# Optimization experiments

Measured on AMD Instinct MI355X. Metric: run time of the kernel, lower is better.

The kernel has to match this reference:

```python
import jax, jax.numpy as jnp
import numpy as np

PS = 16          # patch_size
E = 256          # embed_dim
NH = 4           # num_heads
THR = 1.5        # entropy_threshold (bits)
LN_EPS = 1e-5


def _ln(x, g, b):
    m = x.mean(-1, keepdims=True)
    v = ((x - m) ** 2).mean(-1, keepdims=True)
    return (x - m) / jnp.sqrt(v + LN_EPS) * g + b


def _forward(video, conv_w, conv_b, wq_w, wq_b, wk_w, wk_b, wv_w, wv_b,
             lnq_g, lnq_b, lnk_g, lnk_b, lnv_g, lnv_b,
             in_proj_w, in_proj_b, out_proj_w, out_proj_b,
             dense_w, dense_b, bproj_w, bproj_b, group_query, ent_table):
    # Conv3d(3->E, k=(3,PS,PS), s=(2,PS,PS), p=(1,0,0)) + ReLU
    x = jax.lax.conv_general_dilated(
        video, conv_w, window_strides=(2, PS, PS),
        padding=((1, 1), (0, 0), (0, 0)),
        dimension_numbers=('NCDHW', 'OIDHW', 'NCDHW'))
    x = jax.nn.relu(x + conv_b[None, :, None, None, None])
    B = x.shape[0]
    tokens = x.reshape(B, E, -1).transpose(0, 2, 1)  # [B, N, E]
    N = tokens.shape[1]

    # per-token byte (no_grad in torch)
    byte = jax.lax.stop_gradient(
        jnp.clip(jnp.round(tokens.mean(-1) * 255.0), 0, 255)).astype(jnp.int32)  # [B, N]
    # entropy predictor: probs = softmax(ent_table[last_byte]) (last byte of running seq)
    logits = ent_table[byte[0]]                      # [N, 256]
    p = jax.nn.softmax(logits, axis=-1)
    ent = -(p * jnp.log2(p + 1e-9)).sum(-1)          # [N]
    boundary = (ent > THR).astype(jnp.int32)
    seg = jnp.cumsum(boundary) - boundary            # exclusive cumsum -> segment id per token

    # DecoderCrossAttention with a single shared group_query per segment
    q0 = jnp.broadcast_to(group_query, (B, 1, E))    # byte_representations
    query = _ln(q0 @ wq_w.T + wq_b, lnq_g, lnq_b)    # [B,1,E]
    k = _ln(tokens @ wk_w.T + wk_b, lnk_g, lnk_b)    # [B,N,E]
    v = _ln(tokens @ wv_w.T + wv_b, lnv_g, lnv_b)

    Wqi, Wki, Wvi = in_proj_w[:E], in_proj_w[E:2 * E], in_proj_w[2 * E:]
    bqi, bki, bvi = in_proj_b[:E], in_proj_b[E:2 * E], in_proj_b[2 * E:]
    dh = E // NH
    qp = ((query @ Wqi.T + bqi) * (dh ** -0.5)).reshape(B, NH, dh)  # [B,H,dh]
    kp = (k @ Wki.T + bki).reshape(B, N, NH, dh)
    vp = (v @ Wvi.T + bvi).reshape(B, N, NH, dh)

    scores = jnp.einsum('bhd,bnhd->nbh', qp, kp)     # [N,B,H]
    smax = jax.ops.segment_max(scores, seg, num_segments=N)   # [N,B,H]
    w = jnp.exp(scores - smax[seg])
    denom = jax.ops.segment_sum(w, seg, num_segments=N)       # [N,B,H]
    num = jax.ops.segment_sum(w[..., None] * vp.transpose(1, 0, 2, 3),
                              seg, num_segments=N)            # [N,B,H,dh]
    count = jax.ops.segment_sum(jnp.ones((N,), scores.dtype), seg, num_segments=N)
    valid = count > 0
    safe = jnp.where(valid[:, None, None], denom, 1.0)
    attn = (num / safe[..., None]).transpose(1, 0, 2, 3).reshape(B, N, E)
    out = attn @ out_proj_w.T + out_proj_b
    out = out @ dense_w.T + dense_b
    out = out + q0                                   # residual with byte_representations
    patches = out @ bproj_w.T + bproj_b              # binary_proj
    return jnp.where(valid[None, :, None], patches, 0.0)  # [B, N, E] padded


def setup_inputs() -> dict:
    key = jax.random.key(0)
    ks = jax.random.split(key, 16)
    rn = lambda k, s, sc=0.02: jax.random.normal(k, s, jnp.float32) * sc
    z = lambda *s: jnp.zeros(s, jnp.float32)
    o = lambda *s: jnp.ones(s, jnp.float32)
    return {
        'video': jax.random.normal(ks[0], (4, 3, 32, 224, 224), jnp.float32),
        'conv_w': rn(ks[1], (E, 3, 3, PS, PS)), 'conv_b': z(E),
        'wq_w': rn(ks[2], (E, E)), 'wq_b': z(E),
        'wk_w': rn(ks[3], (E, E)), 'wk_b': z(E),
        'wv_w': rn(ks[4], (E, E)), 'wv_b': z(E),
        'lnq_g': o(E), 'lnq_b': z(E),
        'lnk_g': o(E), 'lnk_b': z(E),
        'lnv_g': o(E), 'lnv_b': z(E),
        'in_proj_w': rn(ks[5], (3 * E, E)), 'in_proj_b': z(3 * E),
        'out_proj_w': rn(ks[6], (E, E)), 'out_proj_b': z(E),
        'dense_w': rn(ks[7], (E, E)), 'dense_b': z(E),
        'bproj_w': rn(ks[8], (E, E)), 'bproj_b': z(E),
        'group_query': jax.random.normal(ks[9], (1, 1, E), jnp.float32),
        'ent_table': jax.random.normal(ks[10], (256, 256), jnp.float32) * 6.0,
    }


def reference(video, conv_w, conv_b, wq_w, wq_b, wk_w, wk_b, wv_w, wv_b,
              lnq_g, lnq_b, lnk_g, lnk_b, lnv_g, lnv_b,
              in_proj_w, in_proj_b, out_proj_w, out_proj_b,
              dense_w, dense_b, bproj_w, bproj_b, group_query, ent_table):
    return _forward(video, conv_w, conv_b, wq_w, wq_b, wk_w, wk_b, wv_w, wv_b,
                    lnq_g, lnq_b, lnk_g, lnk_b, lnv_g, lnv_b,
                    in_proj_w, in_proj_b, out_proj_w, out_proj_b,
                    dense_w, dense_b, bproj_w, bproj_b, group_query, ent_table)
```

## Files before the change

kernel.cpp:

```cpp
#include <hip/hip_runtime.h>
#include <hip/hip_bf16.h>
#include <math.h>

#define NTOK 3136
#define MT 12544
#define KCV 2304
#define THRESH 1.5f
#define LN_EPS 1e-5f

typedef short short8 __attribute__((ext_vector_type(8)));
typedef float f32x4 __attribute__((ext_vector_type(4)));

__device__ __forceinline__ unsigned short f2bf(float f) {
    unsigned int u = __float_as_uint(f);
    u += 0x7fffu + ((u >> 16) & 1u);
    return (unsigned short)(u >> 16);
}
__device__ __forceinline__ float bf2f(unsigned short h) {
    return __uint_as_float(((unsigned int)h) << 16);
}
__device__ __forceinline__ unsigned int cvt_pk_bf16(float x0, float x1) {
    union { __hip_bfloat162 h; unsigned int u; } cv;
    cv.h = __float22bfloat162_rn(make_float2(x0, x1));
    return cv.u;
}
__device__ __forceinline__ void async16(const void* g, void* l) {
    __builtin_amdgcn_global_load_lds((const __attribute__((address_space(1))) void*)g,
                                     (__attribute__((address_space(3))) void*)l, 16, 0, 0);
}

__device__ __forceinline__ float wsum(float v) {
#pragma unroll
    for (int o = 32; o > 0; o >>= 1) v += __shfl_xor(v, o);
    return v;
}
__device__ __forceinline__ float wmax(float v) {
#pragma unroll
    for (int o = 32; o > 0; o >>= 1) v = fmaxf(v, __shfl_xor(v, o));
    return v;
}

__global__ __launch_bounds__(256) void prep_k(
    const float* __restrict__ cw, unsigned short* __restrict__ cwh,
    unsigned short* __restrict__ cwl,
    const float* __restrict__ s0, const float* __restrict__ s1, const float* __restrict__ s2,
    unsigned short* __restrict__ dst,
    const float* __restrict__ gq, const float* __restrict__ wq_w,
    const float* __restrict__ wq_b, const float* __restrict__ lnq_g,
    const float* __restrict__ lnq_b, const float* __restrict__ inW,
    const float* __restrict__ inB, float* __restrict__ qp,
    const float* __restrict__ Wd, const float* __restrict__ Wo,
    const float* __restrict__ bo, const float* __restrict__ bd,
    float* __restrict__ D1, float* __restrict__ tvec)
{
    const int blk = blockIdx.x;
    const int t = threadIdx.x;
    if (blk < 288) {
        int i = blk * 256 + t;
        int e = i & 255, kg = i >> 8;
        const float4* sp = (const float4*)(cw + (size_t)e * KCV + kg * 8);
        float4 x0 = sp[0], x1 = sp[1];
        float av[8] = {x0.x, x0.y, x0.z, x0.w, x1.x, x1.y, x1.z, x1.w};
        short8 hh, ll;
#pragma unroll
        for (int j = 0; j < 8; ++j) {
            unsigned short h = f2bf(av[j]);
            hh[j] = (short)h;
            ll[j] = (short)f2bf(av[j] - bf2f(h));
        }
        size_t off = (size_t)kg * 2048 + e * 8;
        *(short8*)&cwh[off] = hh;
        *(short8*)&cwl[off] = ll;
    } else if (blk < 1568) {
        int i = (blk - 288) * 256 + t;
        if (i >= 327680) return;
        float v;
        if      (i <  65536) v = s0[i];
        else if (i < 131072) v = s1[i - 65536];
        else                 v = s2[i - 131072];
        dst[i] = f2bf(v);
    } else if (blk == 1568) {
        __shared__ float sh[256];
        __shared__ float red[256];
        float acc = wq_b[t];
        for (int j = 0; j < 256; j++) acc += gq[j] * wq_w[t * 256 + j];
        red[t] = acc; __syncthreads();
        for (int o = 128; o > 0; o >>= 1) { if (t < o) red[t] += red[t + o]; __syncthreads(); }
        float m = red[0] * (1.f / 256.f);
        __syncthreads();
        float d = acc - m;
        red[t] = d * d; __syncthreads();
        for (int o = 128; o > 0; o >>= 1) { if (t < o) red[t] += red[t + o]; __syncthreads(); }
        float inv = 1.f / sqrtf(red[0] * (1.f / 256.f) + LN_EPS);
        sh[t] = d * inv * lnq_g[t] + lnq_b[t];
        __syncthreads();
        float a2 = inB[t];
        for (int j = 0; j < 256; j++) a2 += sh[j] * inW[t * 256 + j];
        qp[t] = a2 * 0.125f;
    } else if (blk < 1825) {
        int i = blk - 1569;
        float acc = 0.f;
        for (int k = 0; k < 256; k++) acc += Wd[i * 256 + k] * Wo[k * 256 + t];
        D1[i * 256 + t] = acc;
    } else {
        float acc = bd[t] + gq[t];
        for (int k = 0; k < 256; k++) acc += Wd[t * 256 + k] * bo[k];
        tvec[t] = acc;
    }
}

__global__ __launch_bounds__(256) void prep2_k(
    const float* __restrict__ Wb, const float* __restrict__ D1,
    const float* __restrict__ tvec, const float* __restrict__ bb,
    unsigned short* __restrict__ WcB, float* __restrict__ bc)
{
    const int blk = blockIdx.x;
    const int t = threadIdx.x;
    if (blk < 256) {
        int i = blk;
        float acc = 0.f;
        for (int k = 0; k < 256; k++) acc += Wb[i * 256 + k] * D1[k * 256 + t];
        WcB[i * 256 + t] = f2bf(acc);
    } else {
        float acc = bb[t];
        for (int k = 0; k < 256; k++) acc += Wb[t * 256 + k] * tvec[k];
        bc[t] = acc;
    }
}

__global__ __launch_bounds__(256) void conv_mfma_k(
    const float* __restrict__ video, const unsigned short* __restrict__ cwh,
    const unsigned short* __restrict__ cwl, const float* __restrict__ cbias,
    float* __restrict__ tokmean4, unsigned short* __restrict__ outB)
{
    __shared__ __align__(16) unsigned short Bh[8192], Bl[8192];
    const int t    = threadIdx.x;
    const int lane = t & 63;
    const int w    = t >> 6;
    const int l15  = lane & 15, lq = lane >> 4;
    const int v_  = blockIdx.x;
    const int s_  = (v_ & 7) * 98 + (v_ >> 3);
    const int mb  = s_ >> 2, eb = s_ & 3;
    const int m0  = mb * 64, e0 = eb * 64;

    const int m = m0 + w * 16 + l15;
    const int b = m / NTOK, n = m % NTOK;
    const int d = n / 196, hw = n % 196;
    const int h = hw / 14, ww = hw % 14;
    const float* vb = video + (size_t)(b * 3) * (32 * 50176) + (h * 16) * 224 + ww * 16;
    const int dbase = 2 * d - 1;

    f32x4 acc[4] = {};
    float4 a0, a1, a2, a3, b0, b1, b2, b3;
    short8 rh0, rh1, rl0, rl1;

#define BLOAD(s)                                                                     \
    {                                                                                \
        const size_t g0 = (size_t)((s) * 8 + w) * 2048 + (e0 + lane) * 8;            \
        const size_t g1 = g0 + 4 * 2048;                                             \
        rh0 = *(const short8*)(cwh + g0);                                            \
        rh1 = *(const short8*)(cwh + g1);                                            \
        rl0 = *(const short8*)(cwl + g0);                                            \
        rl1 = *(const short8*)(cwl + g1);                                            \
    }
#define BSTORE(buf)                                                                  \
    {                                                                                \
        const int o = (buf) * 4096 + w * 512 + lane * 8;                             \
        *(short8*)&Bh[o]        = rh0;                                               \
        *(short8*)&Bh[o + 2048] = rh1;                                               \
        *(short8*)&Bl[o]        = rl0;                                               \
        *(short8*)&Bl[o + 2048] = rl1;                                               \
    }
#define LOAD_A32(k0v, x0, x1)                                                        \
    {                                                                                \
        const int k0  = (k0v) + lq * 8;                                              \
        const int c   = k0 / 768;                                                    \
        const int rem = k0 - c * 768;                                                \
        const int kd  = rem >> 8;                                                    \
        const int r2  = rem & 255;                                                   \
        const int id  = dbase + kd;                                                  \
        x0 = make_float4(0.f, 0.f, 0.f, 0.f); x1 = x0;                               \
        if (id >= 0) {                                                               \
            const float* p = vb + (size_t)c * (32 * 50176) + id * 50176 +            \
                             (r2 >> 4) * 224 + (r2 & 15);                            \
            x0 = *(const float4*)p;                                                  \
            x1 = *(const float4*)(p + 4);                                            \
        }                                                                            \
    }
#define CVT_AB(y0, y1, fah, fal)                                                     \
    short8 fah, fal;                                                                 \
    {                                                                                \
        float av[8] = {y0.x, y0.y, y0.z, y0.w, y1.x, y1.y, y1.z, y1.w};              \
        unsigned int ph[4], pl[4];                                                   \
        _Pragma("unroll")                                                            \
        for (int j = 0; j < 4; ++j) {                                                \
            float u0 = av[2 * j], u1 = av[2 * j + 1];                                \
            unsigned int hu = cvt_pk_bf16(u0, u1);                                   \
            float r0 = u0 - __uint_as_float(hu << 16);                               \
            float r1 = u1 - __uint_as_float(hu & 0xffff0000u);                       \
            ph[j] = hu;                                                              \
            pl[j] = cvt_pk_bf16(r0, r1);                                             \
        }                                                                            \
        int4 phv = make_int4(ph[0], ph[1], ph[2], ph[3]);                            \
        int4 plv = make_int4(pl[0], pl[1], pl[2], pl[3]);                            \
        fah = *(short8*)&phv;                                                        \
        fal = *(short8*)&plv;                                                        \
    }

    BLOAD(0);
    LOAD_A32(0, a0, a1);
    LOAD_A32(32, a2, a3);
    BSTORE(0);
    __syncthreads();

    for (int s = 0; s < 36; ++s) {
        const int cbuf = s & 1;
        if (s + 1 < 36) {
            BLOAD(s + 1);
            LOAD_A32((s + 1) * 64,      b0, b1);
            LOAD_A32((s + 1) * 64 + 32, b2, b3);
        }
        {
            CVT_AB(a0, a1, fah, fal);
            const int rb = cbuf * 4096 + lq * 512 + l15 * 8;
#pragma unroll
            for (int ct = 0; ct < 4; ++ct) {
                short8 fbh = *(const short8*)&Bh[rb + ct * 128];
                short8 fbl = *(const short8*)&Bl[rb + ct * 128];
                acc[ct] = __builtin_amdgcn_mfma_f32_16x16x32_bf16(fah, fbh, acc[ct], 0, 0, 0);
                acc[ct] = __builtin_amdgcn_mfma_f32_16x16x32_bf16(fah, fbl, acc[ct], 0, 0, 0);
                acc[ct] = __builtin_amdgcn_mfma_f32_16x16x32_bf16(fal, fbh, acc[ct], 0, 0, 0);
            }
        }
        {
            CVT_AB(a2, a3, fah, fal);
            const int rb = cbuf * 4096 + (4 + lq) * 512 + l15 * 8;
#pragma unroll
            for (int ct = 0; ct < 4; ++ct) {
                short8 fbh = *(const short8*)&Bh[rb + ct * 128];
                short8 fbl = *(const short8*)&Bl[rb + ct * 128];
                acc[ct] = __builtin_amdgcn_mfma_f32_16x16x32_bf16(fah, fbh, acc[ct], 0, 0, 0);
                acc[ct] = __builtin_amdgcn_mfma_f32_16x16x32_bf16(fah, fbl, acc[ct], 0, 0, 0);
                acc[ct] = __builtin_amdgcn_mfma_f32_16x16x32_bf16(fal, fbh, acc[ct], 0, 0, 0);
            }
        }
        if (s + 1 < 36) BSTORE(cbuf ^ 1);
        __syncthreads();
        a0 = b0; a1 = b1; a2 = b2; a3 = b3;
    }
#undef BLOAD
#undef BSTORE
#undef LOAD_A32
#undef CVT_AB

    const int rbase = m0 + w * 16 + lq * 4;
    float rsum[4] = {0.f, 0.f, 0.f, 0.f};
#pragma unroll
    for (int ct = 0; ct < 4; ++ct) {
        int e = e0 + ct * 16 + l15;
        float bias = cbias[e];
#pragma unroll
        for (int r = 0; r < 4; ++r) {
            float vv = fmaxf(acc[ct][r] + bias, 0.f);
            outB[(size_t)(rbase + r) * 256 + e] = f2bf(vv);
            rsum[r] += vv;
        }
    }
    if (m0 < NTOK) {
#pragma unroll
        for (int r = 0; r < 4; ++r) {
            float sv = rsum[r];
            sv += __shfl_xor(sv, 1); sv += __shfl_xor(sv, 2);
            sv += __shfl_xor(sv, 4); sv += __shfl_xor(sv, 8);
            if (l15 == 0) tokmean4[(size_t)eb * NTOK + rbase + r] = sv;
        }
    }
}

__global__ __launch_bounds__(256) void gemm_single_k(
    const unsigned short* __restrict__ A, const unsigned short* __restrict__ W,
    const float* __restrict__ bias, const float* __restrict__ addvec,
    const int* __restrict__ Sptr, float* __restrict__ outF, unsigned short* __restrict__ outB)
{
    __shared__ __align__(16) unsigned short As[8192], Bs[8192];
    const int t = threadIdx.x, lane = t & 63, w = t >> 6;
    const int v_ = blockIdx.x;
    const int s_ = (v_ & 7) * 98 + (v_ >> 3);
    const int m0 = (s_ >> 2) * 64, e0 = (s_ & 3) * 64;
    const int l15 = lane & 15, lq = lane >> 4;
    const unsigned short* ga = A + (size_t)(m0 + lane) * 256;
    const unsigned short* gb = W + (size_t)(e0 + lane) * 256;
#pragma unroll
    for (int kg = w; kg < 16; kg += 4) {
        async16(ga + kg * 8, &As[kg * 512]);
        async16(gb + kg * 8, &Bs[kg * 512]);
    }
    f32x4 acc[4] = {};
    __syncthreads();
#pragma unroll
    for (int s = 0; s < 4; ++s) {
        int kg = s * 4 + lq;
        short8 a = *(const short8*)&As[kg * 512 + (w * 16 + l15) * 8];
#pragma unroll
        for (int ct = 0; ct < 4; ++ct) {
            short8 bb = *(const short8*)&Bs[kg * 512 + (ct * 16 + l15) * 8];
            acc[ct] = __builtin_amdgcn_mfma_f32_16x16x32_bf16(a, bb, acc[ct], 0, 0, 0);
        }
    }
    __syncthreads();
#pragma unroll
    for (int kg = w; kg < 16; kg += 4) {
        async16(ga + (16 + kg) * 8, &As[kg * 512]);
        async16(gb + (16 + kg) * 8, &Bs[kg * 512]);
    }
    __syncthreads();
#pragma unroll
    for (int s = 0; s < 4; ++s) {
        int kg = s * 4 + lq;
        short8 a = *(const short8*)&As[kg * 512 + (w * 16 + l15) * 8];
#pragma unroll
        for (int ct = 0; ct < 4; ++ct) {
            short8 bb = *(const short8*)&Bs[kg * 512 + (ct * 16 + l15) * 8];
            acc[ct] = __builtin_amdgcn_mfma_f32_16x16x32_bf16(a, bb, acc[ct], 0, 0, 0);
        }
    }
    int S = Sptr ? *Sptr : 0x7fffffff;
    int rbase = m0 + w * 16 + lq * 4;
#pragma unroll
    for (int ct = 0; ct < 4; ++ct) {
        int e = e0 + ct * 16 + l15;
        float bv = bias[e] + (addvec ? addvec[e] : 0.f);
#pragma unroll
        for (int r = 0; r < 4; ++r) {
            int mm = rbase + r;
            float vv = acc[ct][r] + bv;
            if ((mm % NTOK) >= S) vv = 0.f;
            size_t off = (size_t)mm * 256 + e;
            if (outF) outF[off] = vv;
            if (outB) outB[off] = f2bf(vv);
        }
    }
}

__global__ __launch_bounds__(256) void gemm_dual_k(
    const unsigned short* __restrict__ A0, const unsigned short* __restrict__ A1,
    const unsigned short* __restrict__ W,
    const float* __restrict__ bias0, const float* __restrict__ bias1,
    unsigned short* __restrict__ outB0, unsigned short* __restrict__ outB1)
{
    __shared__ __align__(16) unsigned short As[8192], Bs[8192];
    const int t = threadIdx.x, lane = t & 63, w = t >> 6;
    const int v_ = blockIdx.x;
    const int s_ = (v_ & 7) * 196 + (v_ >> 3);
    const int mb = s_ >> 3, ebg = s_ & 7;
    const int half = ebg >> 2;
    const unsigned short* A = half ? A1 : A0;
    const float* bias = half ? bias1 : bias0;
    unsigned short* outB = half ? outB1 : outB0;
    const int m0 = mb * 64, eg0 = ebg * 64, el0 = (ebg & 3) * 64;
    const int l15 = lane & 15, lq = lane >> 4;
    const unsigned short* ga = A + (size_t)(m0 + lane) * 256;
    const unsigned short* gb = W + (size_t)(eg0 + lane) * 256;
#pragma unroll
    for (int kg = w; kg < 16; kg += 4) {
        async16(ga + kg * 8, &As[kg * 512]);
        async16(gb + kg * 8, &Bs[kg * 512]);
    }
    f32x4 acc[4] = {};
    __syncthreads();
#pragma unroll
    for (int s = 0; s < 4; ++s) {
        int kg = s * 4 + lq;
        short8 a = *(const short8*)&As[kg * 512 + (w * 16 + l15) * 8];
#pragma unroll
        for (int ct = 0; ct < 4; ++ct) {
            short8 bb = *(const short8*)&Bs[kg * 512 + (ct * 16 + l15) * 8];
            acc[ct] = __builtin_amdgcn_mfma_f32_16x16x32_bf16(a, bb, acc[ct], 0, 0, 0);
        }
    }
    __syncthreads();
#pragma unroll
    for (int kg = w; kg < 16; kg += 4) {
        async16(ga + (16 + kg) * 8, &As[kg * 512]);
        async16(gb + (16 + kg) * 8, &Bs[kg * 512]);
    }
    __syncthreads();
#pragma unroll
    for (int s = 0; s < 4; ++s) {
        int kg = s * 4 + lq;
        short8 a = *(const short8*)&As[kg * 512 + (w * 16 + l15) * 8];
#pragma unroll
        for (int ct = 0; ct < 4; ++ct) {
            short8 bb = *(const short8*)&Bs[kg * 512 + (ct * 16 + l15) * 8];
            acc[ct] = __builtin_amdgcn_mfma_f32_16x16x32_bf16(a, bb, acc[ct], 0, 0, 0);
        }
    }
    int rbase = m0 + w * 16 + lq * 4;
#pragma unroll
    for (int ct = 0; ct < 4; ++ct) {
        int e = el0 + ct * 16 + l15;
        float bv = bias[e];
#pragma unroll
        for (int r = 0; r < 4; ++r) {
            float vv = acc[ct][r] + bv;
            outB[(size_t)(rbase + r) * 256 + e] = f2bf(vv);
        }
    }
}

__global__ __launch_bounds__(256, 2) void gemm_ln_k(
    const unsigned short* __restrict__ A0, const unsigned short* __restrict__ A1,
    const unsigned short* __restrict__ W,
    const float* __restrict__ bias0, const float* __restrict__ bias1,
    const float* __restrict__ g0, const float* __restrict__ b0,
    const float* __restrict__ g1, const float* __restrict__ b1,
    unsigned short* __restrict__ outVp, const float* __restrict__ qp,
    float* __restrict__ sc)
{
    __shared__ __align__(16) unsigned short As[16384], Bs[16384];
    __shared__ float pst[2][4][64];
    __shared__ float rmean[64], rinv[64];
    const int t = threadIdx.x, lane = t & 63, w = t >> 6;
    const int v_ = blockIdx.x;
    const int s_ = (v_ & 7) * 196 + (v_ >> 3);
    const int mb = s_ >> 3, ebg = s_ & 7;
    const int half = ebg >> 2;
    const unsigned short* A = half ? A1 : A0;
    const float* bias = half ? bias1 : bias0;
    const float* lng  = half ? g1 : g0;
    const float* lnb  = half ? b1 : b0;
    const int m0 = mb * 64, eg0 = ebg * 64, el0 = (ebg & 3) * 64;
    const int l15 = lane & 15, lq = lane >> 4;
    const unsigned short* ga = A + (size_t)(m0 + lane) * 256;
    const unsigned short* gb = W + (size_t)(eg0 + lane) * 256;
#pragma unroll
    for (int kg = w; kg < 32; kg += 4) {
        async16(ga + kg * 8, &As[kg * 512]);
        async16(gb + kg * 8, &Bs[kg * 512]);
    }
    __syncthreads();
    {
        float sum = 0.f, sq = 0.f;
#pragma unroll
        for (int k8 = 0; k8 < 8; ++k8) {
            short8 x = *(const short8*)&As[(w * 8 + k8) * 512 + lane * 8];
#pragma unroll
            for (int j = 0; j < 8; ++j) {
                float xv = bf2f((unsigned short)x[j]);
                sum += xv; sq += xv * xv;
            }
        }
        pst[0][w][lane] = sum; pst[1][w][lane] = sq;
    }
    __syncthreads();
    if (w == 0) {
        float s4 = (pst[0][0][lane] + pst[0][1][lane]) + (pst[0][2][lane] + pst[0][3][lane]);
        float q4 = (pst[1][0][lane] + pst[1][1][lane]) + (pst[1][2][lane] + pst[1][3][lane]);
        float mean = s4 * (1.f / 256.f);
        float var  = q4 * (1.f / 256.f) - mean * mean;
        rmean[lane] = mean;
        rinv[lane]  = 1.f / sqrtf(var + LN_EPS);
    }
    __syncthreads();
    const float myMean = rmean[w * 16 + l15];
    const float myInv  = rinv [w * 16 + l15];

    f32x4 acc[4] = {};
#pragma unroll
    for (int s = 0; s < 8; ++s) {
        int kg = s * 4 + lq;
        short8 araw = *(const short8*)&As[kg * 512 + (w * 16 + l15) * 8];
        float4 gA = *(const float4*)&lng[kg * 8];
        float4 gB = *(const float4*)&lng[kg * 8 + 4];
        float4 bA = *(const float4*)&lnb[kg * 8];
        float4 bB = *(const float4*)&lnb[kg * 8 + 4];
        float y[8];
        y[0] = (bf2f((unsigned short)araw[0]) - myMean) * myInv * gA.x + bA.x;
        y[1] = (bf2f((unsigned short)araw[1]) - myMean) * myInv * gA.y + bA.y;
        y[2] = (bf2f((unsigned short)araw[2]) - myMean) * myInv * gA.z + bA.z;
        y[3] = (bf2f((unsigned short)araw[3]) - myMean) * myInv * gA.w + bA.w;
        y[4] = (bf2f((unsigned short)araw[4]) - myMean) * myInv * gB.x + bB.x;
        y[5] = (bf2f((unsigned short)araw[5]) - myMean) * myInv * gB.y + bB.y;
        y[6] = (bf2f((unsigned short)araw[6]) - myMean) * myInv * gB.z + bB.z;
        y[7] = (bf2f((unsigned short)araw[7]) - myMean) * myInv * gB.w + bB.w;
        int4 pk = make_int4(cvt_pk_bf16(y[0], y[1]), cvt_pk_bf16(y[2], y[3]),
                            cvt_pk_bf16(y[4], y[5]), cvt_pk_bf16(y[6], y[7]));
        short8 a = *(short8*)&pk;
#pragma unroll
        for (int ct = 0; ct < 4; ++ct) {
            short8 bb = *(const short8*)&Bs[kg * 512 + (ct * 16 + l15) * 8];
            acc[ct] = __builtin_amdgcn_mfma_f32_16x16x32_bf16(a, bb, acc[ct], 0, 0, 0);
        }
    }
    int rbase = m0 + w * 16 + lq * 4;
    if (half == 0) {
        float sp[4] = {0.f, 0.f, 0.f, 0.f};
#pragma unroll
        for (int ct = 0; ct < 4; ++ct) {
            int e = el0 + ct * 16 + l15;
            float bv = bias[e];
            float qv = qp[e];
#pragma unroll
            for (int r = 0; r < 4; ++r) sp[r] += (acc[ct][r] + bv) * qv;
        }
#pragma unroll
        for (int r = 0; r < 4; ++r) {
            sp[r] += __shfl_xor(sp[r], 1); sp[r] += __shfl_xor(sp[r], 2);
            sp[r] += __shfl_xor(sp[r], 4); sp[r] += __shfl_xor(sp[r], 8);
        }
        if (l15 == 0) {
#pragma unroll
            for (int r = 0; r < 4; ++r) {
                int mm = rbase + r;
                int bb = mm / NTOK, nn = mm % NTOK;
                sc[(bb * 4 + ebg) * NTOK + nn] = sp[r];
            }
        }
    } else {
#pragma unroll
        for (int ct = 0; ct < 4; ++ct) {
            int e = el0 + ct * 16 + l15;
            float bv = bias[e];
#pragma unroll
            for (int r = 0; r < 4; ++r) {
                float vv = acc[ct][r] + bv;
                outVp[(size_t)(rbase + r) * 256 + e] = f2bf(vv);
            }
        }
    }
}

__global__ __launch_bounds__(256) void boundary_k(
    const float* __restrict__ tokmean4, const float* __restrict__ ent_table,
    int* __restrict__ boundary)
{
    int n    = blockIdx.x * 4 + (threadIdx.x >> 6);
    int lane = threadIdx.x & 63;
    float s0 = tokmean4[n];
    float s1 = tokmean4[NTOK + n];
    float s2 = tokmean4[2 * NTOK + n];
    float s3 = tokmean4[3 * NTOK + n];
    float mean = ((s0 + s1) + (s2 + s3)) * (1.f / 256.f);
    float bf = rintf(mean * 255.f);
    bf = fminf(fmaxf(bf, 0.f), 255.f);
    int byte = (int)bf;
    const float4 lg = reinterpret_cast<const float4*>(ent_table + byte * 256)[lane];
    float mx = wmax(fmaxf(fmaxf(lg.x, lg.y), fmaxf(lg.z, lg.w)));
    float e0 = expf(lg.x - mx), e1 = expf(lg.y - mx), e2 = expf(lg.z - mx), e3 = expf(lg.w - mx);
    float z = wsum(e0 + e1 + e2 + e3);
    float iz = 1.f / z;
    float p0 = e0 * iz, p1 = e1 * iz, p2 = e2 * iz, p3 = e3 * iz;
    float ep = -(p0 * log2f(p0 + 1e-9f) + p1 * log2f(p1 + 1e-9f) +
                 p2 * log2f(p2 + 1e-9f) + p3 * log2f(p3 + 1e-9f));
    ep = wsum(ep);
    if (lane == 0) boundary[n] = (ep > THRESH) ? 1 : 0;
}

__global__ __launch_bounds__(256) void scan_k(const int* __restrict__ boundary,
    int* __restrict__ seg_start, int* __restrict__ Sptr)
{
    __shared__ int sums[256];
    const int t = threadIdx.x;
    const int CH = 13;
    int base = t * CH;
    int s = 0;
    for (int i = 0; i < CH; i++) { int n = base + i; if (n < NTOK) s += boundary[n]; }
    sums[t] = s; __syncthreads();
    for (int o = 1; o < 256; o <<= 1) {
        int v = sums[t];
        int u = (t >= o) ? sums[t - o] : 0;
        __syncthreads();
        sums[t] = v + u;
        __syncthreads();
    }
    int run = (t == 0) ? 0 : sums[t - 1];
    if (t == 0) seg_start[0] = 0;
    for (int i = 0; i < CH; i++) {
        int n = base + i;
        if (n >= NTOK) break;
        int v = boundary[n];
        if (n == NTOK - 1) { Sptr[0] = run + 1; seg_start[run + 1] = NTOK; }
        if (v && (n + 1 < NTOK)) seg_start[run + 1] = n + 1;
        run += v;
    }
}

__global__ __launch_bounds__(256) void attn_bf_k(const float* __restrict__ sc,
    const unsigned short* __restrict__ vp, const int* __restrict__ seg_start,
    const int* __restrict__ Sptr, unsigned short* __restrict__ attn)
{
    int s    = blockIdx.x;
    int b    = blockIdx.y;
    int h    = threadIdx.x >> 6;
    int lane = threadIdx.x & 63;
    unsigned short* orow = attn + ((size_t)b * NTOK + s) * 256;
    int S = *Sptr;
    if (s >= S) { orow[h * 64 + lane] = 0; return; }
    int st = seg_start[s], en = seg_start[s + 1];
    const float* scr = sc + (b * 4 + h) * NTOK;
    float m = -1e30f;
    for (int n = st; n < en; n++) m = fmaxf(m, scr[n]);
    float den = 0.f, acc = 0.f;
    const unsigned short* vpb = vp + (size_t)b * NTOK * 256 + h * 64 + lane;
    for (int n = st; n < en; n++) {
        float wgt = expf(scr[n] - m);
        den += wgt;
        acc += wgt * bf2f(vpb[(size_t)n * 256]);
    }
    orow[h * 64 + lane] = f2bf(acc / den);
}

extern "C" void kernel_launch(void* const* d_in, const int* in_sizes, int n_in,
                              void* d_out, int out_size, void* d_ws, size_t ws_size,
                              hipStream_t stream)
{
    const float* video      = (const float*)d_in[0];
    const float* conv_w     = (const float*)d_in[1];
    const float* conv_b     = (const float*)d_in[2];
    const float* wq_w       = (const float*)d_in[3];
    const float* wq_b       = (const float*)d_in[4];
    const float* wk_w       = (const float*)d_in[5];
    const float* wk_b       = (const float*)d_in[6];
    const float* wv_w       = (const float*)d_in[7];
    const float* wv_b       = (const float*)d_in[8];
    const float* lnq_g      = (const float*)d_in[9];
    const float* lnq_b      = (const float*)d_in[10];
    const float* lnk_g      = (const float*)d_in[11];
    const float* lnk_b      = (const float*)d_in[12];
    const float* lnv_g      = (const float*)d_in[13];
    const float* lnv_b      = (const float*)d_in[14];
    const float* in_proj_w  = (const float*)d_in[15];
    const float* in_proj_b  = (const float*)d_in[16];
    const float* out_proj_w = (const float*)d_in[17];
    const float* out_proj_b = (const float*)d_in[18];
    const float* dense_w    = (const float*)d_in[19];
    const float* dense_b    = (const float*)d_in[20];
    const float* bproj_w    = (const float*)d_in[21];
    const float* bproj_b    = (const float*)d_in[22];
    const float* group_q    = (const float*)d_in[23];
    const float* ent_table  = (const float*)d_in[24];
    float* out = (float*)d_out;

    float* tokmean4 = (float*)d_ws;
    unsigned short* Pk  = (unsigned short*)(tokmean4 + 16384);
    unsigned short* Pv  = Pk  + (size_t)MT * 256;
    unsigned short* B1  = Pv  + (size_t)MT * 256;
    unsigned short* B3v = B1  + (size_t)MT * 256;
    unsigned short* cwh = B3v + (size_t)MT * 256;
    unsigned short* cwl = cwh + 256 * KCV;
    unsigned short* wpool = cwl + 256 * KCV;
    float* sc = (float*)(wpool + 524288);
    float* qp = sc + 16 * NTOK;
    int* boundary  = (int*)(qp + 256);
    int* seg_start = boundary + NTOK;
    int* Sp        = seg_start + (NTOK + 1);
    float* D1   = (float*)(Sp + 64);
    float* tvec = D1 + 65536;
    float* bc   = tvec + 256;

    const unsigned short* inpb = wpool + 131072;
    unsigned short* WcB        = wpool + 327680;

    dim3 blk(256);
    prep_k<<<dim3(1826), blk, 0, stream>>>(conv_w, cwh, cwl,
                                           wk_w, wv_w, in_proj_w, wpool,
                                           group_q, wq_w, wq_b, lnq_g, lnq_b,
                                           in_proj_w, in_proj_b, qp,
                                           dense_w, out_proj_w, out_proj_b, dense_b,
                                           D1, tvec);
    prep2_k<<<dim3(257), blk, 0, stream>>>(bproj_w, D1, tvec, bproj_b, WcB, bc);
    conv_mfma_k<<<dim3(784), blk, 0, stream>>>(video, cwh, cwl, conv_b, tokmean4, B1);
    boundary_k<<<dim3(NTOK / 4), blk, 0, stream>>>(tokmean4, ent_table, boundary);
    scan_k<<<dim3(1), blk, 0, stream>>>(boundary, seg_start, Sp);
    gemm_dual_k<<<dim3(1568), blk, 0, stream>>>(B1, B1, wpool, wk_b, wv_b, Pk, Pv);
    gemm_ln_k<<<dim3(1568), blk, 0, stream>>>(Pk, Pv, inpb + 65536,
                                              in_proj_b + 256, in_proj_b + 512,
                                              lnk_g, lnk_b, lnv_g, lnv_b,
                                              B3v, qp, sc);
    attn_bf_k<<<dim3(NTOK, 4), blk, 0, stream>>>(sc, B3v, seg_start, Sp, B1);
    gemm_single_k<<<dim3(784), blk, 0, stream>>>(B1, WcB, bc,
                                                 nullptr, Sp, out, nullptr);
}
```

Measured before the change: 323.0 us.

## Fold small prep, boundary and scan kernels into neighbouring launches

Merges prep2, the entropy-boundary kernel and the scan kernel into extra blocks of conv, gemm_dual and gemm_ln, cutting the launch count from nine to six. gemm_ln halves its B-tile LDS footprint by loading the weight in two K phases with extra barriers, which may raise occupancy. attn_bf now uses a grid-stride loop over segments with fewer blocks and no longer zero-fills rows beyond S, relying on the final gemm masking those rows. The fused blocks add divergent roles inside the kernels and can make the main blocks wait behind slow auxiliary ones.

```diff
diff --git a/kernel.cpp b/kernel.cpp
--- a/kernel.cpp
+++ b/kernel.cpp
@@ -109,32 +109,29 @@
     }
 }
 
-__global__ __launch_bounds__(256) void prep2_k(
+__global__ __launch_bounds__(256) void conv_mfma_k(
+    const float* __restrict__ video, const unsigned short* __restrict__ cwh,
+    const unsigned short* __restrict__ cwl, const float* __restrict__ cbias,
+    float* __restrict__ tokmean4, unsigned short* __restrict__ outB,
     const float* __restrict__ Wb, const float* __restrict__ D1,
     const float* __restrict__ tvec, const float* __restrict__ bb,
     unsigned short* __restrict__ WcB, float* __restrict__ bc)
 {
-    const int blk = blockIdx.x;
-    const int t = threadIdx.x;
-    if (blk < 256) {
-        int i = blk;
-        float acc = 0.f;
-        for (int k = 0; k < 256; k++) acc += Wb[i * 256 + k] * D1[k * 256 + t];
-        WcB[i * 256 + t] = f2bf(acc);
-    } else {
-        float acc = bb[t];
-        for (int k = 0; k < 256; k++) acc += Wb[t * 256 + k] * tvec[k];
-        bc[t] = acc;
-    }
-}
-
-__global__ __launch_bounds__(256) void conv_mfma_k(
-    const float* __restrict__ video, const unsigned short* __restrict__ cwh,
-    const unsigned short* __restrict__ cwl, const float* __restrict__ cbias,
-    float* __restrict__ tokmean4, unsigned short* __restrict__ outB)
-{
     __shared__ __align__(16) unsigned short Bh[8192], Bl[8192];
     const int t    = threadIdx.x;
+    if (blockIdx.x >= 784) {
+        const int pblk = blockIdx.x - 784;
+        if (pblk < 256) {
+            float acc = 0.f;
+            for (int k = 0; k < 256; k++) acc += Wb[pblk * 256 + k] * D1[k * 256 + t];
+            WcB[pblk * 256 + t] = f2bf(acc);
+        } else {
+            float acc = bb[t];
+            for (int k = 0; k < 256; k++) acc += Wb[t * 256 + k] * tvec[k];
+            bc[t] = acc;
+        }
+        return;
+    }
     const int lane = t & 63;
     const int w    = t >> 6;
     const int l15  = lane & 15, lq = lane >> 4;
@@ -346,10 +343,35 @@
     const unsigned short* __restrict__ A0, const unsigned short* __restrict__ A1,
     const unsigned short* __restrict__ W,
     const float* __restrict__ bias0, const float* __restrict__ bias1,
-    unsigned short* __restrict__ outB0, unsigned short* __restrict__ outB1)
+    unsigned short* __restrict__ outB0, unsigned short* __restrict__ outB1,
+    const float* __restrict__ tokmean4, const float* __restrict__ ent_table,
+    int* __restrict__ boundary)
 {
     __shared__ __align__(16) unsigned short As[8192], Bs[8192];
     const int t = threadIdx.x, lane = t & 63, w = t >> 6;
+    if (blockIdx.x >= 1568) {
+        int n = (blockIdx.x - 1568) * 4 + w;
+        float s0 = tokmean4[n];
+        float s1 = tokmean4[NTOK + n];
+        float s2 = tokmean4[2 * NTOK + n];
+        float s3 = tokmean4[3 * NTOK + n];
+        float mean = ((s0 + s1) + (s2 + s3)) * (1.f / 256.f);
+        float bf = rintf(mean * 255.f);
+        bf = fminf(fmaxf(bf, 0.f), 255.f);
+        int byte = (int)bf;
+        const float4 lg = reinterpret_cast<const float4*>(ent_table + byte * 256)[lane];
+        float mx = wmax(fmaxf(fmaxf(lg.x, lg.y), fmaxf(lg.z, lg.w)));
+        float e0 = expf(lg.x - mx), e1 = expf(lg.y - mx);
+        float e2 = expf(lg.z - mx), e3 = expf(lg.w - mx);
+        float z = wsum(e0 + e1 + e2 + e3);
+        float iz = 1.f / z;
+        float p0 = e0 * iz, p1 = e1 * iz, p2 = e2 * iz, p3 = e3 * iz;
+        float ep = -(p0 * log2f(p0 + 1e-9f) + p1 * log2f(p1 + 1e-9f) +
+                     p2 * log2f(p2 + 1e-9f) + p3 * log2f(p3 + 1e-9f));
+        ep = wsum(ep);
+        if (lane == 0) boundary[n] = (ep > THRESH) ? 1 : 0;
+        return;
+    }
     const int v_ = blockIdx.x;
     const int s_ = (v_ & 7) * 196 + (v_ >> 3);
     const int mb = s_ >> 3, ebg = s_ & 7;
@@ -415,12 +437,39 @@
     const float* __restrict__ g0, const float* __restrict__ b0,
     const float* __restrict__ g1, const float* __restrict__ b1,
     unsigned short* __restrict__ outVp, const float* __restrict__ qp,
-    float* __restrict__ sc)
+    float* __restrict__ sc,
+    const int* __restrict__ boundary, int* __restrict__ seg_start, int* __restrict__ Sptr)
 {
-    __shared__ __align__(16) unsigned short As[16384], Bs[16384];
+    __shared__ __align__(16) unsigned short As[16384], Bs[8192];
     __shared__ float pst[2][4][64];
     __shared__ float rmean[64], rinv[64];
+    __shared__ int sums[256];
     const int t = threadIdx.x, lane = t & 63, w = t >> 6;
+    if (blockIdx.x >= 1568) {
+        const int CH = 13;
+        int base = t * CH;
+        int s = 0;
+        for (int i = 0; i < CH; i++) { int n = base + i; if (n < NTOK) s += boundary[n]; }
+        sums[t] = s; __syncthreads();
+        for (int o = 1; o < 256; o <<= 1) {
+            int v = sums[t];
+            int u = (t >= o) ? sums[t - o] : 0;
+            __syncthreads();
+            sums[t] = v + u;
+            __syncthreads();
+        }
+        int run = (t == 0) ? 0 : sums[t - 1];
+        if (t == 0) seg_start[0] = 0;
+        for (int i = 0; i < CH; i++) {
+            int n = base + i;
+            if (n >= NTOK) break;
+            int v = boundary[n];
+            if (n == NTOK - 1) { Sptr[0] = run + 1; seg_start[run + 1] = NTOK; }
+            if (v && (n + 1 < NTOK)) seg_start[run + 1] = n + 1;
+            run += v;
+        }
+        return;
+    }
     const int v_ = blockIdx.x;
     const int s_ = (v_ & 7) * 196 + (v_ >> 3);
     const int mb = s_ >> 3, ebg = s_ & 7;
@@ -434,10 +483,9 @@
     const unsigned short* ga = A + (size_t)(m0 + lane) * 256;
     const unsigned short* gb = W + (size_t)(eg0 + lane) * 256;
 #pragma unroll
-    for (int kg = w; kg < 32; kg += 4) {
-        async16(ga + kg * 8, &As[kg * 512]);
-        async16(gb + kg * 8, &Bs[kg * 512]);
-    }
+    for (int kg = w; kg < 32; kg += 4) async16(ga + kg * 8, &As[kg * 512]);
+#pragma unroll
+    for (int kg = w; kg < 16; kg += 4) async16(gb + kg * 8, &Bs[kg * 512]);
     __syncthreads();
     {
         float sum = 0.f, sq = 0.f;
@@ -467,29 +515,39 @@
 
     f32x4 acc[4] = {};
 #pragma unroll
-    for (int s = 0; s < 8; ++s) {
-        int kg = s * 4 + lq;
-        short8 araw = *(const short8*)&As[kg * 512 + (w * 16 + l15) * 8];
-        float4 gA = *(const float4*)&lng[kg * 8];
-        float4 gB = *(const float4*)&lng[kg * 8 + 4];
-        float4 bA = *(const float4*)&lnb[kg * 8];
-        float4 bB = *(const float4*)&lnb[kg * 8 + 4];
-        float y[8];
-        y[0] = (bf2f((unsigned short)araw[0]) - myMean) * myInv * gA.x + bA.x;
-        y[1] = (bf2f((unsigned short)araw[1]) - myMean) * myInv * gA.y + bA.y;
-        y[2] = (bf2f((unsigned short)araw[2]) - myMean) * myInv * gA.z + bA.z;
-        y[3] = (bf2f((unsigned short)araw[3]) - myMean) * myInv * gA.w + bA.w;
-        y[4] = (bf2f((unsigned short)araw[4]) - myMean) * myInv * gB.x + bB.x;
-        y[5] = (bf2f((unsigned short)araw[5]) - myMean) * myInv * gB.y + bB.y;
-        y[6] = (bf2f((unsigned short)araw[6]) - myMean) * myInv * gB.z + bB.z;
-        y[7] = (bf2f((unsigned short)araw[7]) - myMean) * myInv * gB.w + bB.w;
-        int4 pk = make_int4(cvt_pk_bf16(y[0], y[1]), cvt_pk_bf16(y[2], y[3]),
-                            cvt_pk_bf16(y[4], y[5]), cvt_pk_bf16(y[6], y[7]));
-        short8 a = *(short8*)&pk;
-#pragma unroll
-        for (int ct = 0; ct < 4; ++ct) {
-            short8 bb = *(const short8*)&Bs[kg * 512 + (ct * 16 + l15) * 8];
-            acc[ct] = __builtin_amdgcn_mfma_f32_16x16x32_bf16(a, bb, acc[ct], 0, 0, 0);
+    for (int ph = 0; ph < 2; ++ph) {
+        if (ph == 1) {
+            __syncthreads();
+#pragma unroll
+            for (int kg = w; kg < 16; kg += 4) async16(gb + (16 + kg) * 8, &Bs[kg * 512]);
+            __syncthreads();
+        }
+#pragma unroll
+        for (int s = 0; s < 4; ++s) {
+            int kg = ph * 16 + s * 4 + lq;
+            short8 araw = *(const short8*)&As[kg * 512 + (w * 16 + l15) * 8];
+            float4 gA = *(const float4*)&lng[kg * 8];
+            float4 gB = *(const float4*)&lng[kg * 8 + 4];
+            float4 bA = *(const float4*)&lnb[kg * 8];
+            float4 bB = *(const float4*)&lnb[kg * 8 + 4];
+            float y[8];
+            y[0] = (bf2f((unsigned short)araw[0]) - myMean) * myInv * gA.x + bA.x;
+            y[1] = (bf2f((unsigned short)araw[1]) - myMean) * myInv * gA.y + bA.y;
+            y[2] = (bf2f((unsigned short)araw[2]) - myMean) * myInv * gA.z + bA.z;
+            y[3] = (bf2f((unsigned short)araw[3]) - myMean) * myInv * gA.w + bA.w;
+            y[4] = (bf2f((unsigned short)araw[4]) - myMean) * myInv * gB.x + bB.x;
+            y[5] = (bf2f((unsigned short)araw[5]) - myMean) * myInv * gB.y + bB.y;
+            y[6] = (bf2f((unsigned short)araw[6]) - myMean) * myInv * gB.z + bB.z;
+            y[7] = (bf2f((unsigned short)araw[7]) - myMean) * myInv * gB.w + bB.w;
+            int4 pk = make_int4(cvt_pk_bf16(y[0], y[1]), cvt_pk_bf16(y[2], y[3]),
+                                cvt_pk_bf16(y[4], y[5]), cvt_pk_bf16(y[6], y[7]));
+            short8 a = *(short8*)&pk;
+            const int bkg = s * 4 + lq;
+#pragma unroll
+            for (int ct = 0; ct < 4; ++ct) {
+                short8 bb = *(const short8*)&Bs[bkg * 512 + (ct * 16 + l15) * 8];
+                acc[ct] = __builtin_amdgcn_mfma_f32_16x16x32_bf16(a, bb, acc[ct], 0, 0, 0);
+            }
         }
     }
     int rbase = m0 + w * 16 + lq * 4;
@@ -530,84 +588,28 @@
     }
 }
 
-__global__ __launch_bounds__(256) void boundary_k(
-    const float* __restrict__ tokmean4, const float* __restrict__ ent_table,
-    int* __restrict__ boundary)
-{
-    int n    = blockIdx.x * 4 + (threadIdx.x >> 6);
-    int lane = threadIdx.x & 63;
-    float s0 = tokmean4[n];
-    float s1 = tokmean4[NTOK + n];
-    float s2 = tokmean4[2 * NTOK + n];
-    float s3 = tokmean4[3 * NTOK + n];
-    float mean = ((s0 + s1) + (s2 + s3)) * (1.f / 256.f);
-    float bf = rintf(mean * 255.f);
-    bf = fminf(fmaxf(bf, 0.f), 255.f);
-    int byte = (int)bf;
-    const float4 lg = reinterpret_cast<const float4*>(ent_table + byte * 256)[lane];
-    float mx = wmax(fmaxf(fmaxf(lg.x, lg.y), fmaxf(lg.z, lg.w)));
-    float e0 = expf(lg.x - mx), e1 = expf(lg.y - mx), e2 = expf(lg.z - mx), e3 = expf(lg.w - mx);
-    float z = wsum(e0 + e1 + e2 + e3);
-    float iz = 1.f / z;
-    float p0 = e0 * iz, p1 = e1 * iz, p2 = e2 * iz, p3 = e3 * iz;
-    float ep = -(p0 * log2f(p0 + 1e-9f) + p1 * log2f(p1 + 1e-9f) +
-                 p2 * log2f(p2 + 1e-9f) + p3 * log2f(p3 + 1e-9f));
-    ep = wsum(ep);
-    if (lane == 0) boundary[n] = (ep > THRESH) ? 1 : 0;
-}
-
-__global__ __launch_bounds__(256) void scan_k(const int* __restrict__ boundary,
-    int* __restrict__ seg_start, int* __restrict__ Sptr)
-{
-    __shared__ int sums[256];
-    const int t = threadIdx.x;
-    const int CH = 13;
-    int base = t * CH;
-    int s = 0;
-    for (int i = 0; i < CH; i++) { int n = base + i; if (n < NTOK) s += boundary[n]; }
-    sums[t] = s; __syncthreads();
-    for (int o = 1; o < 256; o <<= 1) {
-        int v = sums[t];
-        int u = (t >= o) ? sums[t - o] : 0;
-        __syncthreads();
-        sums[t] = v + u;
-        __syncthreads();
-    }
-    int run = (t == 0) ? 0 : sums[t - 1];
-    if (t == 0) seg_start[0] = 0;
-    for (int i = 0; i < CH; i++) {
-        int n = base + i;
-        if (n >= NTOK) break;
-        int v = boundary[n];
-        if (n == NTOK - 1) { Sptr[0] = run + 1; seg_start[run + 1] = NTOK; }
-        if (v && (n + 1 < NTOK)) seg_start[run + 1] = n + 1;
-        run += v;
-    }
-}
-
 __global__ __launch_bounds__(256) void attn_bf_k(const float* __restrict__ sc,
     const unsigned short* __restrict__ vp, const int* __restrict__ seg_start,
     const int* __restrict__ Sptr, unsigned short* __restrict__ attn)
 {
-    int s    = blockIdx.x;
     int b    = blockIdx.y;
     int h    = threadIdx.x >> 6;
     int lane = threadIdx.x & 63;
-    unsigned short* orow = attn + ((size_t)b * NTOK + s) * 256;
     int S = *Sptr;
-    if (s >= S) { orow[h * 64 + lane] = 0; return; }
-    int st = seg_start[s], en = seg_start[s + 1];
-    const float* scr = sc + (b * 4 + h) * NTOK;
-    float m = -1e30f;
-    for (int n = st; n < en; n++) m = fmaxf(m, scr[n]);
-    float den = 0.f, acc = 0.f;
-    const unsigned short* vpb = vp + (size_t)b * NTOK * 256 + h * 64 + lane;
-    for (int n = st; n < en; n++) {
-        float wgt = expf(scr[n] - m);
-        den += wgt;
-        acc += wgt * bf2f(vpb[(size_t)n * 256]);
-    }
-    orow[h * 64 + lane] = f2bf(acc / den);
+    const unsigned short* vpb0 = vp + (size_t)b * NTOK * 256 + h * 64 + lane;
+    for (int s = blockIdx.x; s < S; s += gridDim.x) {
+        int st = seg_start[s], en = seg_start[s + 1];
+        const float* scr = sc + (b * 4 + h) * NTOK;
+        float m = -1e30f;
+        for (int n = st; n < en; n++) m = fmaxf(m, scr[n]);
+        float den = 0.f, acc = 0.f;
+        for (int n = st; n < en; n++) {
+            float wgt = expf(scr[n] - m);
+            den += wgt;
+            acc += wgt * bf2f(vpb0[(size_t)n * 256]);
+        }
+        attn[((size_t)b * NTOK + s) * 256 + h * 64 + lane] = f2bf(acc / den);
+    }
 }
 
 extern "C" void kernel_launch(void* const* d_in, const int* in_sizes, int n_in,
@@ -668,16 +670,16 @@
                                            in_proj_w, in_proj_b, qp,
                                            dense_w, out_proj_w, out_proj_b, dense_b,
                                            D1, tvec);
-    prep2_k<<<dim3(257), blk, 0, stream>>>(bproj_w, D1, tvec, bproj_b, WcB, bc);
-    conv_mfma_k<<<dim3(784), blk, 0, stream>>>(video, cwh, cwl, conv_b, tokmean4, B1);
-    boundary_k<<<dim3(NTOK / 4), blk, 0, stream>>>(tokmean4, ent_table, boundary);
-    scan_k<<<dim3(1), blk, 0, stream>>>(boundary, seg_start, Sp);
-    gemm_dual_k<<<dim3(1568), blk, 0, stream>>>(B1, B1, wpool, wk_b, wv_b, Pk, Pv);
-    gemm_ln_k<<<dim3(1568), blk, 0, stream>>>(Pk, Pv, inpb + 65536,
+    conv_mfma_k<<<dim3(1041), blk, 0, stream>>>(video, cwh, cwl, conv_b, tokmean4, B1,
+                                                bproj_w, D1, tvec, bproj_b, WcB, bc);
+    gemm_dual_k<<<dim3(2352), blk, 0, stream>>>(B1, B1, wpool, wk_b, wv_b, Pk, Pv,
+                                                tokmean4, ent_table, boundary);
+    gemm_ln_k<<<dim3(1569), blk, 0, stream>>>(Pk, Pv, inpb + 65536,
                                               in_proj_b + 256, in_proj_b + 512,
                                               lnk_g, lnk_b, lnv_g, lnv_b,
-                                              B3v, qp, sc);
-    attn_bf_k<<<dim3(NTOK, 4), blk, 0, stream>>>(sc, B3v, seg_start, Sp, B1);
+                                              B3v, qp, sc,
+                                              boundary, seg_start, Sp);
+    attn_bf_k<<<dim3(512, 4), blk, 0, stream>>>(sc, B3v, seg_start, Sp, B1);
     gemm_single_k<<<dim3(784), blk, 0, stream>>>(B1, WcB, bc,
                                                  nullptr, Sp, out, nullptr);
 }
```

Measured after the change: 300.2 us. -7.1%, faster.
